# Kernel optimization log

Measured on AMD Instinct MI355X. Metric: run time of the kernel, lower is better.

Reference implementation:

```python
import jax, jax.numpy as jnp
import numpy as np

B, N, D = 16, 2048, 64

def setup_inputs() -> dict:
    key = jax.random.key(0)
    kq, kk, kv = jax.random.split(key, 3)
    queries = jax.random.normal(kq, (B, N, D), dtype=jnp.float32)
    keys = jax.random.normal(kk, (B, N, D), dtype=jnp.float32)
    values = jax.random.normal(kv, (B, N, D), dtype=jnp.float32)
    scaling_factor = jnp.asarray(np.sqrt(D), dtype=jnp.float32)
    return {"queries": queries, "keys": keys, "values": values, "scaling_factor": scaling_factor}

def reference(queries, keys, values, scaling_factor):
    # scores: [B, N, N] = Q K^T / scale
    scores = jnp.einsum('bqd,bkd->bqk', queries, keys) / scaling_factor
    atn = jax.nn.softmax(scores, axis=2)
    return jnp.einsum('bqk,bkd->bqd', atn, values)
```

## Files before the change

kernel.cpp:

```cpp
#include <hip/hip_runtime.h>
#include <hip/hip_bf16.h>

#define BATCH 16
#define SEQ 2048
#define DIM 64
#define TQ 64
#define KT 128
#define KP 72
#define VPP 136
#define PP 136

typedef __attribute__((ext_vector_type(8))) __bf16 bf16x8;
typedef __attribute__((ext_vector_type(8))) unsigned short u16x8;
typedef __attribute__((ext_vector_type(16))) float f32x16;

#if __has_builtin(__builtin_amdgcn_exp2f)
#define EXP2F(x) __builtin_amdgcn_exp2f(x)
#else
#define EXP2F(x) __expf(0.69314718055994531f * (x))
#endif

__device__ __forceinline__ unsigned short f2bf(float f) {
    union { float f; unsigned int u; } v; v.f = f;
    unsigned int r = v.u + 0x7fffu + ((v.u >> 16) & 1u);
    return (unsigned short)(r >> 16);
}

__device__ __forceinline__ unsigned short f2bf_hw(float f) {
    __bf16 h = (__bf16)f;
    return __builtin_bit_cast(unsigned short, h);
}

__device__ __forceinline__ bf16x8 ld_bf8(const unsigned short* p) {
    u16x8 u = *(const u16x8*)p;
    return __builtin_bit_cast(bf16x8, u);
}

__global__ __launch_bounds__(256)
void preconvert_all(const float* __restrict__ Q, const float* __restrict__ K,
                    const float* __restrict__ V, const float* __restrict__ scaling,
                    unsigned short* __restrict__ Qs, unsigned short* __restrict__ Ks,
                    unsigned short* __restrict__ Vts) {
    const int tid = threadIdx.x;
    if (blockIdx.x < 1024) {
        const float c = 1.4426950408889634f / scaling[0];
        const size_t i = ((size_t)blockIdx.x * 256 + tid) * 8;
        float4 a0 = *(const float4*)(Q + i);
        float4 a1 = *(const float4*)(Q + i + 4);
        u16x8 qo;
        qo[0] = f2bf(a0.x * c); qo[1] = f2bf(a0.y * c); qo[2] = f2bf(a0.z * c); qo[3] = f2bf(a0.w * c);
        qo[4] = f2bf(a1.x * c); qo[5] = f2bf(a1.y * c); qo[6] = f2bf(a1.z * c); qo[7] = f2bf(a1.w * c);
        *(u16x8*)(Qs + i) = qo;
        float4 b0 = *(const float4*)(K + i);
        float4 b1 = *(const float4*)(K + i + 4);
        u16x8 ko;
        ko[0] = f2bf(b0.x); ko[1] = f2bf(b0.y); ko[2] = f2bf(b0.z); ko[3] = f2bf(b0.w);
        ko[4] = f2bf(b1.x); ko[5] = f2bf(b1.y); ko[6] = f2bf(b1.z); ko[7] = f2bf(b1.w);
        *(u16x8*)(Ks + i) = ko;
    } else {
        __shared__ float vt[KT * 65];
        const int vb = blockIdx.x - 1024;
        const int b  = vb >> 4;
        const int kt = (vb & 15) * KT;
        const float* src = V + ((size_t)(b * SEQ + kt)) * DIM;
        #pragma unroll
        for (int p = 0; p < 8; ++p) {
            const int f = p * 256 + tid;
            const int row = f >> 4, c4 = (f & 15) << 2;
            float4 x = *(const float4*)(src + row * DIM + c4);
            vt[row * 65 + c4 + 0] = x.x; vt[row * 65 + c4 + 1] = x.y;
            vt[row * 65 + c4 + 2] = x.z; vt[row * 65 + c4 + 3] = x.w;
        }
        __syncthreads();
        #pragma unroll
        for (int p = 0; p < 4; ++p) {
            const int cid = p * 256 + tid;
            const int d = cid >> 4, kc = cid & 15;
            u16x8 o;
            #pragma unroll
            for (int j = 0; j < 8; ++j) o[j] = f2bf(vt[(kc * 8 + j) * 65 + d]);
            *(u16x8*)(Vts + ((size_t)(b * DIM + d)) * SEQ + kt + kc * 8) = o;
        }
    }
}

__global__ __launch_bounds__(128, 2)
void attn_flash_kernel(const unsigned short* __restrict__ Qs,
                       const unsigned short* __restrict__ Ks,
                       const unsigned short* __restrict__ Vts,
                       float* __restrict__ O) {
    __shared__ unsigned short Klds[KT * KP];
    __shared__ unsigned short Vtlds[DIM * VPP];
    __shared__ unsigned short Plds[2 * 32 * PP];

    const int tid  = threadIdx.x;
    const int w    = tid >> 6;
    const int lane = tid & 63;
    const int m    = lane & 31;
    const int h    = lane >> 5;

    const int b  = blockIdx.x >> 5;
    const int q0 = (blockIdx.x & 31) * TQ;

    bf16x8 aq[4];
    {
        const unsigned short* qsrc = Qs + ((size_t)(b * SEQ + q0 + w * 32 + m)) * DIM;
        #pragma unroll
        for (int c = 0; c < 4; ++c) aq[c] = ld_bf8(qsrc + c * 16 + h * 8);
    }

    f32x16 Oacc[2];
    #pragma unroll
    for (int dt = 0; dt < 2; ++dt)
        #pragma unroll
        for (int r = 0; r < 16; ++r) Oacc[dt][r] = 0.f;
    float psum[16];
    #pragma unroll
    for (int r = 0; r < 16; ++r) psum[r] = 0.f;

    unsigned short* pw = &Plds[w * 32 * PP];

    for (int kt = 0; kt < SEQ; kt += KT) {
        __syncthreads();
        {
            const unsigned short* kbase = Ks + ((size_t)(b * SEQ + kt)) * DIM;
            #pragma unroll
            for (int p = 0; p < 8; ++p) {
                const int cid = p * 128 + tid;
                const int key = cid >> 3, ch = cid & 7;
                *(u16x8*)&Klds[key * KP + ch * 8] = *(const u16x8*)(kbase + key * DIM + ch * 8);
            }
        }
        {
            const unsigned short* vbase = Vts + (size_t)b * DIM * SEQ + kt;
            #pragma unroll
            for (int p = 0; p < 8; ++p) {
                const int cid = p * 128 + tid;
                const int d = cid >> 4, ch = cid & 15;
                *(u16x8*)&Vtlds[d * VPP + ch * 8] = *(const u16x8*)(vbase + (size_t)d * SEQ + ch * 8);
            }
        }
        __syncthreads();

        #pragma unroll
        for (int t = 0; t < 4; ++t) {
            f32x16 S;
            #pragma unroll
            for (int r = 0; r < 16; ++r) S[r] = 0.f;
            #pragma unroll
            for (int c = 0; c < 4; ++c) {
                bf16x8 bk = ld_bf8(&Klds[(t * 32 + m) * KP + c * 16 + h * 8]);
                S = __builtin_amdgcn_mfma_f32_32x32x16_bf16(aq[c], bk, S, 0, 0, 0);
            }
            #pragma unroll
            for (int r = 0; r < 16; ++r) {
                float p = EXP2F(S[r]);
                psum[r] += p;
                const int row = (r & 3) + 8 * (r >> 2) + 4 * h;
                pw[row * PP + t * 32 + m] = f2bf_hw(p);
            }
        }

        #pragma unroll
        for (int kc = 0; kc < 8; ++kc) {
            bf16x8 pa = ld_bf8(&pw[m * PP + kc * 16 + h * 8]);
            #pragma unroll
            for (int dt = 0; dt < 2; ++dt) {
                bf16x8 bv = ld_bf8(&Vtlds[(dt * 32 + m) * VPP + kc * 16 + h * 8]);
                Oacc[dt] = __builtin_amdgcn_mfma_f32_32x32x16_bf16(pa, bv, Oacc[dt], 0, 0, 0);
            }
        }
    }

    #pragma unroll
    for (int r = 0; r < 16; ++r) {
        float l = psum[r];
        #pragma unroll
        for (int off = 1; off < 32; off <<= 1) l += __shfl_xor(l, off);
        const float invl = 1.0f / l;
        const int row = (r & 3) + 8 * (r >> 2) + 4 * h;
        float* orow = O + ((size_t)(b * SEQ + q0 + w * 32 + row)) * DIM;
        #pragma unroll
        for (int dt = 0; dt < 2; ++dt)
            orow[dt * 32 + m] = Oacc[dt][r] * invl;
    }
}

extern "C" void kernel_launch(void* const* d_in, const int* in_sizes, int n_in,
                              void* d_out, int out_size, void* d_ws, size_t ws_size,
                              hipStream_t stream) {
    const float* Q = (const float*)d_in[0];
    const float* K = (const float*)d_in[1];
    const float* V = (const float*)d_in[2];
    const float* scaling = (const float*)d_in[3];
    float* O = (float*)d_out;

    const size_t NELEM = (size_t)BATCH * SEQ * DIM;
    unsigned short* Qs  = (unsigned short*)d_ws;
    unsigned short* Ks  = Qs + NELEM;
    unsigned short* Vts = Ks + NELEM;

    preconvert_all<<<dim3(1024 + BATCH * (SEQ / KT)), dim3(256), 0, stream>>>(Q, K, V, scaling, Qs, Ks, Vts);
    attn_flash_kernel<<<dim3(BATCH * (SEQ / TQ)), dim3(128), 0, stream>>>(Qs, Ks, Vts, O);
}
```

Before: 122.1 us.

## Split keys across warps, keep P in registers, async LDS loads, fold Q conversion

Q conversion now happens inside the attention kernel, and the preconvert kernel only handles K and V, writing them in an MFMA-friendly pre-swizzled tile layout. The attention kernel runs 4 warps: two key-halves times two query halves. Each warp streams its own K or V tile into LDS with global_load_lds async copies. The P matrix now stays in registers through lane shuffles and swapped MFMA operands, so the LDS round trip for P is gone, and the two key-half partials are merged through LDS at the end. The aim is to cut launch and conversion traffic, LDS traffic and synchronisation, at the cost of 64KB dynamic shared memory per block, which may limit occupancy.

```diff
diff --git a/kernel.cpp b/kernel.cpp
--- a/kernel.cpp
+++ b/kernel.cpp
@@ -4,14 +4,10 @@
 #define BATCH 16
 #define SEQ 2048
 #define DIM 64
-#define TQ 64
-#define KT 128
-#define KP 72
-#define VPP 136
-#define PP 136
 
 typedef __attribute__((ext_vector_type(8))) __bf16 bf16x8;
 typedef __attribute__((ext_vector_type(8))) unsigned short u16x8;
+typedef __attribute__((ext_vector_type(4))) unsigned int u32x4;
 typedef __attribute__((ext_vector_type(16))) float f32x16;
 
 #if __has_builtin(__builtin_amdgcn_exp2f)
@@ -20,48 +16,37 @@
 #define EXP2F(x) __expf(0.69314718055994531f * (x))
 #endif
 
-__device__ __forceinline__ unsigned short f2bf(float f) {
-    union { float f; unsigned int u; } v; v.f = f;
-    unsigned int r = v.u + 0x7fffu + ((v.u >> 16) & 1u);
-    return (unsigned short)(r >> 16);
-}
-
 __device__ __forceinline__ unsigned short f2bf_hw(float f) {
     __bf16 h = (__bf16)f;
     return __builtin_bit_cast(unsigned short, h);
 }
 
+__device__ __forceinline__ unsigned int pk_bf16(float lo, float hi) {
+    unsigned int a = f2bf_hw(lo), b = f2bf_hw(hi);
+    return a | (b << 16);
+}
+
 __device__ __forceinline__ bf16x8 ld_bf8(const unsigned short* p) {
     u16x8 u = *(const u16x8*)p;
     return __builtin_bit_cast(bf16x8, u);
 }
 
+__device__ __forceinline__ void async_copy16(const unsigned short* g, unsigned short* l) {
+    __builtin_amdgcn_global_load_lds(
+        (const __attribute__((address_space(1))) unsigned int*)g,
+        (__attribute__((address_space(3))) unsigned int*)l, 16, 0, 0);
+}
+
 __global__ __launch_bounds__(256)
-void preconvert_all(const float* __restrict__ Q, const float* __restrict__ K,
-                    const float* __restrict__ V, const float* __restrict__ scaling,
-                    unsigned short* __restrict__ Qs, unsigned short* __restrict__ Ks,
-                    unsigned short* __restrict__ Vts) {
+void preconvert_kv(const float* __restrict__ K, const float* __restrict__ V,
+                   unsigned short* __restrict__ Ks, unsigned short* __restrict__ Vts) {
+    __shared__ float vt[128 * 65];
     const int tid = threadIdx.x;
-    if (blockIdx.x < 1024) {
-        const float c = 1.4426950408889634f / scaling[0];
-        const size_t i = ((size_t)blockIdx.x * 256 + tid) * 8;
-        float4 a0 = *(const float4*)(Q + i);
-        float4 a1 = *(const float4*)(Q + i + 4);
-        u16x8 qo;
-        qo[0] = f2bf(a0.x * c); qo[1] = f2bf(a0.y * c); qo[2] = f2bf(a0.z * c); qo[3] = f2bf(a0.w * c);
-        qo[4] = f2bf(a1.x * c); qo[5] = f2bf(a1.y * c); qo[6] = f2bf(a1.z * c); qo[7] = f2bf(a1.w * c);
-        *(u16x8*)(Qs + i) = qo;
-        float4 b0 = *(const float4*)(K + i);
-        float4 b1 = *(const float4*)(K + i + 4);
-        u16x8 ko;
-        ko[0] = f2bf(b0.x); ko[1] = f2bf(b0.y); ko[2] = f2bf(b0.z); ko[3] = f2bf(b0.w);
-        ko[4] = f2bf(b1.x); ko[5] = f2bf(b1.y); ko[6] = f2bf(b1.z); ko[7] = f2bf(b1.w);
-        *(u16x8*)(Ks + i) = ko;
-    } else {
-        __shared__ float vt[KT * 65];
-        const int vb = blockIdx.x - 1024;
-        const int b  = vb >> 4;
-        const int kt = (vb & 15) * KT;
+    const int b = blockIdx.x >> 4;
+    const int t = blockIdx.x & 15;
+    const int kt = t * 128;
+
+    {
         const float* src = V + ((size_t)(b * SEQ + kt)) * DIM;
         #pragma unroll
         for (int p = 0; p < 8; ++p) {
@@ -71,42 +56,75 @@
             vt[row * 65 + c4 + 0] = x.x; vt[row * 65 + c4 + 1] = x.y;
             vt[row * 65 + c4 + 2] = x.z; vt[row * 65 + c4 + 3] = x.w;
         }
-        __syncthreads();
+    }
+    {
+        const float* src = K + ((size_t)(b * SEQ + kt)) * DIM;
+        unsigned short* dst = Ks + ((size_t)(b * 16 + t)) * 8192;
         #pragma unroll
         for (int p = 0; p < 4; ++p) {
             const int cid = p * 256 + tid;
-            const int d = cid >> 4, kc = cid & 15;
+            const int key = cid >> 3, g = cid & 7;
+            const int d0 = (g >> 1) * 16 + (g & 1) * 8;
+            float4 x0 = *(const float4*)(src + key * DIM + d0);
+            float4 x1 = *(const float4*)(src + key * DIM + d0 + 4);
             u16x8 o;
-            #pragma unroll
-            for (int j = 0; j < 8; ++j) o[j] = f2bf(vt[(kc * 8 + j) * 65 + d]);
-            *(u16x8*)(Vts + ((size_t)(b * DIM + d)) * SEQ + kt + kc * 8) = o;
-        }
-    }
-}
-
-__global__ __launch_bounds__(128, 2)
-void attn_flash_kernel(const unsigned short* __restrict__ Qs,
+            o[0] = f2bf_hw(x0.x); o[1] = f2bf_hw(x0.y); o[2] = f2bf_hw(x0.z); o[3] = f2bf_hw(x0.w);
+            o[4] = f2bf_hw(x1.x); o[5] = f2bf_hw(x1.y); o[6] = f2bf_hw(x1.z); o[7] = f2bf_hw(x1.w);
+            *(u16x8*)(dst + (g * 128 + key) * 8) = o;
+        }
+    }
+    __syncthreads();
+    {
+        unsigned short* dst = Vts + ((size_t)(b * 16 + t)) * 8192;
+        #pragma unroll
+        for (int p = 0; p < 4; ++p) {
+            const int cid = p * 256 + tid;
+            const int g = cid >> 6, d = cid & 63;
+            const int k0 = (g >> 1) * 16 + (g & 1) * 8;
+            u16x8 o;
+            #pragma unroll
+            for (int j = 0; j < 8; ++j) o[j] = f2bf_hw(vt[(k0 + j) * 65 + d]);
+            *(u16x8*)(dst + (g * 64 + d) * 8) = o;
+        }
+    }
+}
+
+__global__ __launch_bounds__(256, 2)
+void attn_flash_kernel(const float* __restrict__ Q,
                        const unsigned short* __restrict__ Ks,
                        const unsigned short* __restrict__ Vts,
+                       const float* __restrict__ scaling,
                        float* __restrict__ O) {
-    __shared__ unsigned short Klds[KT * KP];
-    __shared__ unsigned short Vtlds[DIM * VPP];
-    __shared__ unsigned short Plds[2 * 32 * PP];
+    extern __shared__ char smem[];
+    unsigned short* lds = (unsigned short*)smem;
 
     const int tid  = threadIdx.x;
     const int w    = tid >> 6;
     const int lane = tid & 63;
     const int m    = lane & 31;
     const int h    = lane >> 5;
+    const int qw   = w & 1;
+    const int kw   = w >> 1;
 
     const int b  = blockIdx.x >> 5;
-    const int q0 = (blockIdx.x & 31) * TQ;
+    const int q0 = (blockIdx.x & 31) * 64;
+
+    const float csc = 1.4426950408889634f / scaling[0];
 
     bf16x8 aq[4];
     {
-        const unsigned short* qsrc = Qs + ((size_t)(b * SEQ + q0 + w * 32 + m)) * DIM;
-        #pragma unroll
-        for (int c = 0; c < 4; ++c) aq[c] = ld_bf8(qsrc + c * 16 + h * 8);
+        const float* qsrc = Q + ((size_t)(b * SEQ + q0 + qw * 32 + m)) * DIM + h * 8;
+        #pragma unroll
+        for (int c = 0; c < 4; ++c) {
+            float4 x0 = *(const float4*)(qsrc + c * 16);
+            float4 x1 = *(const float4*)(qsrc + c * 16 + 4);
+            u32x4 pk;
+            pk[0] = pk_bf16(x0.x * csc, x0.y * csc);
+            pk[1] = pk_bf16(x0.z * csc, x0.w * csc);
+            pk[2] = pk_bf16(x1.x * csc, x1.y * csc);
+            pk[3] = pk_bf16(x1.z * csc, x1.w * csc);
+            aq[c] = __builtin_bit_cast(bf16x8, pk);
+        }
     }
 
     f32x16 Oacc[2];
@@ -114,32 +132,19 @@
     for (int dt = 0; dt < 2; ++dt)
         #pragma unroll
         for (int r = 0; r < 16; ++r) Oacc[dt][r] = 0.f;
-    float psum[16];
-    #pragma unroll
-    for (int r = 0; r < 16; ++r) psum[r] = 0.f;
-
-    unsigned short* pw = &Plds[w * 32 * PP];
-
-    for (int kt = 0; kt < SEQ; kt += KT) {
+    float psum = 0.f;
+
+    unsigned short* Kt = lds + kw * 16384;
+    unsigned short* Vt = lds + kw * 16384 + 8192;
+    const unsigned short* gsrc = ((w & 1) ? Vts : Ks) + ((size_t)(b * 16 + kw * 8)) * 8192;
+    unsigned short* ldst = lds + w * 8192;
+
+    for (int it = 0; it < 8; ++it) {
         __syncthreads();
-        {
-            const unsigned short* kbase = Ks + ((size_t)(b * SEQ + kt)) * DIM;
-            #pragma unroll
-            for (int p = 0; p < 8; ++p) {
-                const int cid = p * 128 + tid;
-                const int key = cid >> 3, ch = cid & 7;
-                *(u16x8*)&Klds[key * KP + ch * 8] = *(const u16x8*)(kbase + key * DIM + ch * 8);
-            }
-        }
-        {
-            const unsigned short* vbase = Vts + (size_t)b * DIM * SEQ + kt;
-            #pragma unroll
-            for (int p = 0; p < 8; ++p) {
-                const int cid = p * 128 + tid;
-                const int d = cid >> 4, ch = cid & 15;
-                *(u16x8*)&Vtlds[d * VPP + ch * 8] = *(const u16x8*)(vbase + (size_t)d * SEQ + ch * 8);
-            }
-        }
+        const unsigned short* gt = gsrc + (size_t)it * 8192;
+        #pragma unroll
+        for (int j = 0; j < 16; ++j)
+            async_copy16(gt + j * 512 + lane * 8, ldst + j * 512);
         __syncthreads();
 
         #pragma unroll
@@ -149,40 +154,70 @@
             for (int r = 0; r < 16; ++r) S[r] = 0.f;
             #pragma unroll
             for (int c = 0; c < 4; ++c) {
-                bf16x8 bk = ld_bf8(&Klds[(t * 32 + m) * KP + c * 16 + h * 8]);
-                S = __builtin_amdgcn_mfma_f32_32x32x16_bf16(aq[c], bk, S, 0, 0, 0);
-            }
-            #pragma unroll
-            for (int r = 0; r < 16; ++r) {
-                float p = EXP2F(S[r]);
-                psum[r] += p;
-                const int row = (r & 3) + 8 * (r >> 2) + 4 * h;
-                pw[row * PP + t * 32 + m] = f2bf_hw(p);
-            }
-        }
-
-        #pragma unroll
-        for (int kc = 0; kc < 8; ++kc) {
-            bf16x8 pa = ld_bf8(&pw[m * PP + kc * 16 + h * 8]);
-            #pragma unroll
-            for (int dt = 0; dt < 2; ++dt) {
-                bf16x8 bv = ld_bf8(&Vtlds[(dt * 32 + m) * VPP + kc * 16 + h * 8]);
-                Oacc[dt] = __builtin_amdgcn_mfma_f32_32x32x16_bf16(pa, bv, Oacc[dt], 0, 0, 0);
-            }
-        }
-    }
-
-    #pragma unroll
-    for (int r = 0; r < 16; ++r) {
-        float l = psum[r];
-        #pragma unroll
-        for (int off = 1; off < 32; off <<= 1) l += __shfl_xor(l, off);
-        const float invl = 1.0f / l;
-        const int row = (r & 3) + 8 * (r >> 2) + 4 * h;
-        float* orow = O + ((size_t)(b * SEQ + q0 + w * 32 + row)) * DIM;
+                bf16x8 bk = ld_bf8(&Kt[((c * 2 + h) * 128 + t * 32 + m) * 8]);
+                S = __builtin_amdgcn_mfma_f32_32x32x16_bf16(bk, aq[c], S, 0, 0, 0);
+            }
+            unsigned int d0[8], ds[8];
+            float ps = 0.f;
+            #pragma unroll
+            for (int k = 0; k < 4; ++k) {
+                float p0 = EXP2F(S[4 * k + 0]);
+                float p1 = EXP2F(S[4 * k + 1]);
+                float p2 = EXP2F(S[4 * k + 2]);
+                float p3 = EXP2F(S[4 * k + 3]);
+                ps += (p0 + p1) + (p2 + p3);
+                d0[2 * k + 0] = pk_bf16(p0, p1);
+                d0[2 * k + 1] = pk_bf16(p2, p3);
+            }
+            psum += ps;
+            #pragma unroll
+            for (int i = 0; i < 8; ++i) ds[i] = (unsigned int)__shfl_xor((int)d0[i], 32);
+            #pragma unroll
+            for (int c2 = 0; c2 < 2; ++c2) {
+                u32x4 bw;
+                bw[0] = h ? ds[4 * c2 + 2] : d0[4 * c2 + 0];
+                bw[1] = h ? ds[4 * c2 + 3] : d0[4 * c2 + 1];
+                bw[2] = h ? d0[4 * c2 + 2] : ds[4 * c2 + 0];
+                bw[3] = h ? d0[4 * c2 + 3] : ds[4 * c2 + 1];
+                bf16x8 pb = __builtin_bit_cast(bf16x8, bw);
+                const int kc = 2 * t + c2;
+                #pragma unroll
+                for (int dt = 0; dt < 2; ++dt) {
+                    bf16x8 bv = ld_bf8(&Vt[((kc * 2 + h) * 64 + dt * 32 + m) * 8]);
+                    Oacc[dt] = __builtin_amdgcn_mfma_f32_32x32x16_bf16(bv, pb, Oacc[dt], 0, 0, 0);
+                }
+            }
+        }
+    }
+
+    float lhalf = psum + __shfl_xor(psum, 32);
+    __syncthreads();
+    float* fl = (float*)smem;
+    if (kw == 1) {
+        float* dst = fl + (w - 2) * 2112 + lane * 33;
         #pragma unroll
         for (int dt = 0; dt < 2; ++dt)
-            orow[dt * 32 + m] = Oacc[dt][r] * invl;
+            #pragma unroll
+            for (int r = 0; r < 16; ++r) dst[dt * 16 + r] = Oacc[dt][r];
+        dst[32] = lhalf;
+    }
+    __syncthreads();
+    if (kw == 0) {
+        const float* pr = fl + w * 2112 + lane * 33;
+        const float invl = 1.0f / (lhalf + pr[32]);
+        float* orow = O + ((size_t)(b * SEQ + q0 + qw * 32 + m)) * DIM;
+        #pragma unroll
+        for (int dt = 0; dt < 2; ++dt) {
+            #pragma unroll
+            for (int k = 0; k < 4; ++k) {
+                float4 o4;
+                o4.x = (Oacc[dt][4 * k + 0] + pr[dt * 16 + 4 * k + 0]) * invl;
+                o4.y = (Oacc[dt][4 * k + 1] + pr[dt * 16 + 4 * k + 1]) * invl;
+                o4.z = (Oacc[dt][4 * k + 2] + pr[dt * 16 + 4 * k + 2]) * invl;
+                o4.w = (Oacc[dt][4 * k + 3] + pr[dt * 16 + 4 * k + 3]) * invl;
+                *(float4*)(orow + dt * 32 + 8 * k + 4 * h) = o4;
+            }
+        }
     }
 }
 
@@ -195,11 +230,9 @@
     const float* scaling = (const float*)d_in[3];
     float* O = (float*)d_out;
 
-    const size_t NELEM = (size_t)BATCH * SEQ * DIM;
-    unsigned short* Qs  = (unsigned short*)d_ws;
-    unsigned short* Ks  = Qs + NELEM;
-    unsigned short* Vts = Ks + NELEM;
-
-    preconvert_all<<<dim3(1024 + BATCH * (SEQ / KT)), dim3(256), 0, stream>>>(Q, K, V, scaling, Qs, Ks, Vts);
-    attn_flash_kernel<<<dim3(BATCH * (SEQ / TQ)), dim3(128), 0, stream>>>(Qs, Ks, Vts, O);
-}
+    unsigned short* Ks  = (unsigned short*)d_ws;
+    unsigned short* Vts = Ks + (size_t)BATCH * 16 * 8192;
+
+    preconvert_kv<<<dim3(BATCH * 16), dim3(256), 0, stream>>>(K, V, Ks, Vts);
+    attn_flash_kernel<<<dim3(BATCH * (SEQ / 64)), dim3(256), 65536, stream>>>(Q, Ks, Vts, scaling, O);
+}
```

Result: faster. 108.2 us (-11.4%).
